# Performance work log

Hardware: AMD Instinct MI355X
Metric: run time of the kernel (lower is better)

The kernel has to match this reference:

```python
import jax, jax.numpy as jnp
import numpy as np

VOXEL_SCALE = 20.0   # cfg.SPARSE3D.VOXEL_SCALE (metric -> voxel pixels)
POOLER_SCALE = 0.25  # cfg.MODEL.ROI_BOX_HEAD.POOLER_SCALES_SPATIAL[0]
RES = 7              # pooler resolution per axis
EPS = 1e-5           # BatchNorm eps


def _roi_align_3d(feat, boxes_px, batch_idx, res):
    """3D ROIAlign, sampling_ratio=1 (one trilinear sample per bin).
    feat: [B, X, Y, Z, C] channels-last; boxes_px: [N,6] = (x1,y1,z1,x2,y2,z2)
    in feature-map coordinates. Returns [N, C, res, res, res]."""
    B, X, Y, Z, C = feat.shape
    N = boxes_px.shape[0]
    start, end = boxes_px[:, :3], boxes_px[:, 3:]
    size = jnp.maximum(end - start, 1.0)            # [N,3] legacy min roi size
    binsz = size / res
    off = jnp.arange(res, dtype=boxes_px.dtype) + 0.5
    px = start[:, 0:1] + off[None, :] * binsz[:, 0:1]   # [N,res]
    py = start[:, 1:2] + off[None, :] * binsz[:, 1:2]
    pz = start[:, 2:3] + off[None, :] * binsz[:, 2:3]
    P = res * res * res
    PX = jnp.broadcast_to(px[:, :, None, None], (N, res, res, res)).reshape(N, P)
    PY = jnp.broadcast_to(py[:, None, :, None], (N, res, res, res)).reshape(N, P)
    PZ = jnp.broadcast_to(pz[:, None, None, :], (N, res, res, res)).reshape(N, P)

    def corners(p, dim):
        p0 = jnp.floor(p)
        frac = p - p0
        i0 = jnp.clip(p0.astype(jnp.int32), 0, dim - 1)
        i1 = jnp.clip(p0.astype(jnp.int32) + 1, 0, dim - 1)
        return i0, i1, frac

    x0, x1, lx = corners(PX, X)
    y0, y1, ly = corners(PY, Y)
    z0, z1, lz = corners(PZ, Z)
    feat_flat = feat.reshape(B * X * Y * Z, C)
    base = batch_idx.astype(jnp.int32)[:, None]          # [N,1]
    acc = jnp.zeros((N, P, C), feat.dtype)
    for dx in (0, 1):  # 8 trilinear corners; fixed small loop
        xi, wx = (x0, 1.0 - lx) if dx == 0 else (x1, lx)
        for dy in (0, 1):
            yi, wy = (y0, 1.0 - ly) if dy == 0 else (y1, ly)
            for dz in (0, 1):
                zi, wz = (z0, 1.0 - lz) if dz == 0 else (z1, lz)
                lin = ((base * X + xi) * Y + yi) * Z + zi  # [N,P]
                acc = acc + (wx * wy * wz)[:, :, None] * feat_flat[lin]
    pooled = acc.reshape(N, res, res, res, C)  # 1 sample per bin -> no avg
    return pooled.transpose(0, 4, 1, 2, 3)     # [N, C, rx, ry, rz]


def setup_inputs():
    key = jax.random.key(0)
    ks = jax.random.split(key, 8)
    B, C, X, Y, Z = 2, 128, 80, 80, 20
    N, rep = 1024, 128 * RES              # rep = OUT_CHANNELS * pooler_z = 896
    in_size = C * RES * RES * RES         # 43904
    features = jax.random.normal(ks[0], (B, X, Y, Z, C), jnp.float32)
    ext = jnp.array([16.0, 16.0, 4.0], jnp.float32)  # metric extent = dim/(voxel_scale*pooler_scale)
    ctr = jax.random.uniform(ks[1], (N, 3), jnp.float32) * ext
    half = 0.25 + jax.random.uniform(ks[2], (N, 3), jnp.float32) * 1.75
    boxes = jnp.concatenate([ctr - half, ctr + half], axis=1)  # metric units
    batch_idx = jax.random.randint(ks[3], (N,), 0, B, jnp.int32)
    conv_w = jax.random.normal(ks[4], (rep, C, RES), jnp.float32) * 0.02
    conv_b = jnp.zeros((rep,), jnp.float32)
    gamma = jnp.ones((rep,), jnp.float32)
    beta = jnp.zeros((rep,), jnp.float32)
    fc6_w = jax.random.normal(ks[5], (in_size, rep), jnp.float32) * np.float32(1.0 / np.sqrt(in_size))
    fc6_b = jnp.zeros((rep,), jnp.float32)
    fc7_w = jax.random.normal(ks[6], (rep, rep), jnp.float32) * np.float32(1.0 / np.sqrt(rep))
    fc7_b = jnp.zeros((rep,), jnp.float32)
    return dict(features=features, boxes=boxes, conv_w=conv_w, conv_b=conv_b,
                gamma=gamma, beta=beta, fc6_w=fc6_w, fc6_b=fc6_b,
                fc7_w=fc7_w, fc7_b=fc7_b, batch_idx=batch_idx)


def reference(features, boxes, conv_w, conv_b, gamma, beta,
              fc6_w, fc6_b, fc7_w, fc7_b, batch_idx):
    # convert_metric_to_pixel (x voxel_scale) fused with pooler spatial scale
    boxes_px = boxes * (VOXEL_SCALE * POOLER_SCALE)
    pooled = _roi_align_3d(features, boxes_px, batch_idx, RES)  # [N,C,7,7,7]
    # conv3d kernel [1,1,Z]: contract channels and z -> [N, rep, 7, 7]
    y = jnp.einsum('ncxyz,rcz->nrxy', pooled, conv_w) + conv_b[None, :, None, None]
    # BatchNorm3d, training-mode batch statistics per channel
    mu = y.mean(axis=(0, 2, 3), keepdims=True)
    var = ((y - mu) ** 2).mean(axis=(0, 2, 3), keepdims=True)
    y = (y - mu) * jax.lax.rsqrt(var + EPS) * gamma[None, :, None, None] + beta[None, :, None, None]
    y = jax.nn.relu(y)
    x2 = y.reshape(y.shape[0], -1)                   # [N, rep*49] == [N, C*343]
    x3 = jax.nn.relu(x2 @ fc6_w + fc6_b)
    x4 = jax.nn.relu(x3 @ fc7_w + fc7_b)
    return x4
```

## Files before the change

kernel.cpp:

```cpp
#include <hip/hip_runtime.h>
#include <cstdint>

typedef unsigned short u16;
using bf16x8  = __attribute__((ext_vector_type(8))) __bf16;
using floatx4 = __attribute__((ext_vector_type(4))) float;

__device__ __forceinline__ u16 f2bf(float f) {
    uint32_t u = __builtin_bit_cast(uint32_t, f);
    u += 0x7fffu + ((u >> 16) & 1u);
    return (u16)(u >> 16);
}
__device__ __forceinline__ float bf2f(u16 h) {
    uint32_t u = ((uint32_t)h) << 16;
    return __builtin_bit_cast(float, u);
}

__global__ __launch_bounds__(256) void k_roialign(
    const float* __restrict__ feat, const float* __restrict__ boxes,
    const int* __restrict__ bidx, u16* __restrict__ A1)
{
    const int n = blockIdx.x;
    const int t = threadIdx.x;
    const float s = 5.0f;
    const float x1 = boxes[n*6+0]*s, y1 = boxes[n*6+1]*s, z1 = boxes[n*6+2]*s;
    const float x2 = boxes[n*6+3]*s, y2 = boxes[n*6+4]*s, z2 = boxes[n*6+5]*s;
    const float binx = fmaxf(x2-x1, 1.0f) * (1.0f/7.0f);
    const float biny = fmaxf(y2-y1, 1.0f) * (1.0f/7.0f);
    const float binz = fmaxf(z2-z1, 1.0f) * (1.0f/7.0f);
    const int b = bidx[n];
    const float* fb = feat + (size_t)b * 80 * 80 * 20 * 128;
    const int c4   = (t & 31) * 4;
    const int slot = t >> 5;

    for (int p = slot; p < 343; p += 8) {
        const int xq = p / 49;
        const int rem = p - xq * 49;
        const int yq = rem / 7;
        const int zq = rem - yq * 7;
        const float px = x1 + ((float)xq + 0.5f) * binx;
        const float py = y1 + ((float)yq + 0.5f) * biny;
        const float pz = z1 + ((float)zq + 0.5f) * binz;
        const float fx = floorf(px), fy = floorf(py), fz = floorf(pz);
        const float lx = px - fx, ly = py - fy, lz = pz - fz;
        const int xi0 = min(max((int)fx,     0), 79);
        const int xi1 = min(max((int)fx + 1, 0), 79);
        const int yi0 = min(max((int)fy,     0), 79);
        const int yi1 = min(max((int)fy + 1, 0), 79);
        const int zi0 = min(max((int)fz,     0), 19);
        const int zi1 = min(max((int)fz + 1, 0), 19);
        const float wx0 = 1.f-lx, wy0 = 1.f-ly, wz0 = 1.f-lz;
        const float w00 = wx0*wy0, w01 = wx0*ly, w10 = lx*wy0, w11 = lx*ly;
        float a0=0.f, a1=0.f, a2=0.f, a3=0.f;
#define RC(W, XI, YI, ZI) { \
        const float4 v = *(const float4*)(fb + (size_t)(((XI)*80+(YI))*20+(ZI))*128 + c4); \
        a0 = fmaf((W), v.x, a0); a1 = fmaf((W), v.y, a1); \
        a2 = fmaf((W), v.z, a2); a3 = fmaf((W), v.w, a3); }
        RC(w00*wz0, xi0, yi0, zi0); RC(w00*lz, xi0, yi0, zi1);
        RC(w01*wz0, xi0, yi1, zi0); RC(w01*lz, xi0, yi1, zi1);
        RC(w10*wz0, xi1, yi0, zi0); RC(w10*lz, xi1, yi0, zi1);
        RC(w11*wz0, xi1, yi1, zi0); RC(w11*lz, xi1, yi1, zi1);
#undef RC
        const int m = n * 49 + xq * 7 + yq;
        ushort4 o;
        o.x = f2bf(a0); o.y = f2bf(a1); o.z = f2bf(a2); o.w = f2bf(a3);
        *(ushort4*)(A1 + (size_t)m * 896 + zq * 128 + c4) = o;
    }
}

__global__ __launch_bounds__(256) void k_prep_wc(
    const float* __restrict__ w, u16* __restrict__ out)
{
    const int i = blockIdx.x * 256 + threadIdx.x;
    const int r = i / 896, k = i % 896;
    const int z = k >> 7, c = k & 127;
    out[i] = f2bf(w[(r * 128 + c) * 7 + z]);
}

template <int PERM>
__global__ __launch_bounds__(256) void k_transpose(
    const float* __restrict__ in, u16* __restrict__ out, int Kin)
{
    __shared__ u16 tile[64][72];
    const int kp0 = blockIdx.x * 64, r0 = blockIdx.y * 64;
    const int t = threadIdx.x;
#pragma unroll
    for (int it = 0; it < 16; ++it) {
        const int idx = it * 256 + t;
        const int i = idx >> 6, rl = idx & 63;
        const int kp = kp0 + i;
        const int k = PERM ? (kp % 896) * 49 + (kp / 896) : kp;
        tile[i][rl] = f2bf(in[(size_t)k * 896 + r0 + rl]);
    }
    __syncthreads();
#pragma unroll
    for (int it = 0; it < 16; ++it) {
        const int idx = it * 256 + t;
        const int rl = idx >> 6, i = idx & 63;
        out[(size_t)(r0 + rl) * Kin + kp0 + i] = tile[i][rl];
    }
}

template <int EPI>
__global__ __launch_bounds__(256) void k_gemm(
    const u16* __restrict__ A, const u16* __restrict__ Bt,
    float* __restrict__ outF, u16* __restrict__ outH,
    const float* __restrict__ bias, float* __restrict__ bnsum, float* __restrict__ bnsq,
    int Astride, int Bstride, int kpc, int ktot, int partStride)
{
    __shared__ __align__(16) u16 lA[128 * 40];
    __shared__ __align__(16) u16 lB[128 * 40];
    const int t = threadIdx.x;
    const int wave = t >> 6, lane = t & 63;
    const int wm = wave & 1, wn = wave >> 1;
    const int quad = lane >> 4, lr = lane & 15;
    const size_t m0 = (size_t)blockIdx.x * 128;
    const size_t n0 = (size_t)blockIdx.y * 128;
    const int kbeg = blockIdx.z * kpc;
    const int kend = min(kbeg + kpc, ktot);

    floatx4 acc[4][4];
    const floatx4 zero = {0.f, 0.f, 0.f, 0.f};
#pragma unroll
    for (int a = 0; a < 4; ++a)
#pragma unroll
        for (int bq = 0; bq < 4; ++bq) acc[a][bq] = zero;

    const int e0 = t * 8;
    const int r0s = e0 >> 5, c0s = e0 & 31;
    const int e1 = e0 + 2048;
    const int r1s = e1 >> 5, c1s = e1 & 31;
    const u16* Ab = A + m0 * (size_t)Astride;
    const u16* Bb = Bt + n0 * (size_t)Bstride;

    for (int ks = kbeg; ks < kend; ++ks) {
        const size_t k0 = (size_t)ks * 32;
        const uint4 va0 = *(const uint4*)(Ab + (size_t)r0s * Astride + k0 + c0s);
        const uint4 va1 = *(const uint4*)(Ab + (size_t)r1s * Astride + k0 + c1s);
        const uint4 vb0 = *(const uint4*)(Bb + (size_t)r0s * Bstride + k0 + c0s);
        const uint4 vb1 = *(const uint4*)(Bb + (size_t)r1s * Bstride + k0 + c1s);
        __syncthreads();
        *(uint4*)(lA + r0s * 40 + c0s) = va0;
        *(uint4*)(lA + r1s * 40 + c1s) = va1;
        *(uint4*)(lB + r0s * 40 + c0s) = vb0;
        *(uint4*)(lB + r1s * 40 + c1s) = vb1;
        __syncthreads();
        bf16x8 af[4], bfr[4];
#pragma unroll
        for (int mt = 0; mt < 4; ++mt)
            af[mt] = *(const bf16x8*)(lA + (wm * 64 + mt * 16 + lr) * 40 + quad * 8);
#pragma unroll
        for (int nt = 0; nt < 4; ++nt)
            bfr[nt] = *(const bf16x8*)(lB + (wn * 64 + nt * 16 + lr) * 40 + quad * 8);
#pragma unroll
        for (int mt = 0; mt < 4; ++mt)
#pragma unroll
            for (int nt = 0; nt < 4; ++nt)
                acc[mt][nt] = __builtin_amdgcn_mfma_f32_16x16x32_bf16(
                    af[mt], bfr[nt], acc[mt][nt], 0, 0, 0);
    }

    if (EPI == 0) {
#pragma unroll
        for (int nt = 0; nt < 4; ++nt) {
            const int n = (int)n0 + wn * 64 + nt * 16 + lr;
            const float bv = bias[n];
            float s1 = 0.f, s2 = 0.f;
#pragma unroll
            for (int mt = 0; mt < 4; ++mt) {
#pragma unroll
                for (int j = 0; j < 4; ++j) {
                    const int m = (int)m0 + wm * 64 + mt * 16 + quad * 4 + j;
                    const float v = acc[mt][nt][j] + bv;
                    outH[(size_t)m * 896 + n] = f2bf(v);
                    s1 += v;
                    s2 = fmaf(v, v, s2);
                }
            }
            s1 += __shfl_xor(s1, 16); s1 += __shfl_xor(s1, 32);
            s2 += __shfl_xor(s2, 16); s2 += __shfl_xor(s2, 32);
            if (quad == 0) {
                atomicAdd(&bnsum[n], s1);
                atomicAdd(&bnsq[n],  s2);
            }
        }
    } else {
        float* po = outF + (size_t)blockIdx.z * partStride;
#pragma unroll
        for (int nt = 0; nt < 4; ++nt) {
            const int n = (int)n0 + wn * 64 + nt * 16 + lr;
#pragma unroll
            for (int mt = 0; mt < 4; ++mt) {
#pragma unroll
                for (int j = 0; j < 4; ++j) {
                    const int m = (int)m0 + wm * 64 + mt * 16 + quad * 4 + j;
                    po[(size_t)m * 896 + n] = acc[mt][nt][j];
                }
            }
        }
    }
}

__global__ __launch_bounds__(256) void k_bn_apply(
    u16* __restrict__ y, const float* __restrict__ s1, const float* __restrict__ s2,
    const float* __restrict__ gamma, const float* __restrict__ beta)
{
    const size_t i = ((size_t)blockIdx.x * 256 + threadIdx.x) * 8;
    uint4 d = *(const uint4*)(y + i);
    const u16* h = (const u16*)&d;
    const int r0 = (int)(i % 896);
    __align__(16) u16 o[8];
    const float invM = 1.0f / 50176.0f;
#pragma unroll
    for (int j = 0; j < 8; ++j) {
        const int r = r0 + j;
        const float mu  = s1[r] * invM;
        const float var = fmaf(-mu, mu, s2[r] * invM);
        const float rs  = rsqrtf(var + 1e-5f);
        const float v   = (bf2f(h[j]) - mu) * rs * gamma[r] + beta[r];
        o[j] = f2bf(fmaxf(v, 0.f));
    }
    *(uint4*)(y + i) = *(const uint4*)o;
}

__global__ __launch_bounds__(256) void k_x3(
    const float* __restrict__ part, const float* __restrict__ bias, u16* __restrict__ x3)
{
    const size_t i = ((size_t)blockIdx.x * 256 + threadIdx.x) * 4;
    float a0=0.f, a1=0.f, a2=0.f, a3=0.f;
#pragma unroll
    for (int c = 0; c < 16; ++c) {
        const float4 v = *(const float4*)(part + (size_t)c * 917504 + i);
        a0 += v.x; a1 += v.y; a2 += v.z; a3 += v.w;
    }
    const int r = (int)(i % 896);
    ushort4 o;
    o.x = f2bf(fmaxf(a0 + bias[r+0], 0.f));
    o.y = f2bf(fmaxf(a1 + bias[r+1], 0.f));
    o.z = f2bf(fmaxf(a2 + bias[r+2], 0.f));
    o.w = f2bf(fmaxf(a3 + bias[r+3], 0.f));
    *(ushort4*)(x3 + i) = o;
}

__global__ __launch_bounds__(256) void k_out(
    const float* __restrict__ part, const float* __restrict__ bias, float* __restrict__ out)
{
    const size_t i = ((size_t)blockIdx.x * 256 + threadIdx.x) * 4;
    float a0=0.f, a1=0.f, a2=0.f, a3=0.f;
#pragma unroll
    for (int c = 0; c < 4; ++c) {
        const float4 v = *(const float4*)(part + (size_t)c * 917504 + i);
        a0 += v.x; a1 += v.y; a2 += v.z; a3 += v.w;
    }
    const int r = (int)(i % 896);
    float4 o;
    o.x = fmaxf(a0 + bias[r+0], 0.f);
    o.y = fmaxf(a1 + bias[r+1], 0.f);
    o.z = fmaxf(a2 + bias[r+2], 0.f);
    o.w = fmaxf(a3 + bias[r+3], 0.f);
    *(float4*)(out + i) = o;
}

extern "C" void kernel_launch(void* const* d_in, const int* in_sizes, int n_in,
                              void* d_out, int out_size, void* d_ws, size_t ws_size,
                              hipStream_t stream)
{
    (void)in_sizes; (void)n_in; (void)out_size; (void)ws_size;
    const float* features = (const float*)d_in[0];
    const float* boxes    = (const float*)d_in[1];
    const float* conv_w   = (const float*)d_in[2];
    const float* conv_b   = (const float*)d_in[3];
    const float* gamma    = (const float*)d_in[4];
    const float* beta     = (const float*)d_in[5];
    const float* fc6_w    = (const float*)d_in[6];
    const float* fc6_b    = (const float*)d_in[7];
    const float* fc7_w    = (const float*)d_in[8];
    const float* fc7_b    = (const float*)d_in[9];
    const int*   batch_idx = (const int*)d_in[10];
    float* out = (float*)d_out;
    char* ws = (char*)d_ws;

    size_t off = 0;
    auto alloc = [&](size_t b) { size_t o = off; off += (b + 255) & ~(size_t)255; return o; };
    const size_t oA1   = alloc(50176ull * 896 * 2);
    const size_t oWcT  = alloc(896ull * 896 * 2);
    const size_t oY    = alloc(50176ull * 896 * 2);
    const size_t oF6T  = alloc(43904ull * 896 * 2);
    const size_t oF7T  = alloc(896ull * 896 * 2);
    const size_t oStat = alloc(8192);
    const size_t oP2 = oA1;
    const size_t oX3 = oA1 + 58720256;
    const size_t oP3 = oX3 + 1835008;

    u16*   A1    = (u16*)(ws + oA1);
    u16*   WcT   = (u16*)(ws + oWcT);
    u16*   Y     = (u16*)(ws + oY);
    u16*   F6T   = (u16*)(ws + oF6T);
    u16*   F7T   = (u16*)(ws + oF7T);
    float* bnsum = (float*)(ws + oStat);
    float* bnsq  = bnsum + 1024;
    float* P2    = (float*)(ws + oP2);
    u16*   X3    = (u16*)(ws + oX3);
    float* P3    = (float*)(ws + oP3);

    k_prep_wc<<<3136, 256, 0, stream>>>(conv_w, WcT);
    k_transpose<1><<<dim3(686, 14), 256, 0, stream>>>(fc6_w, F6T, 43904);
    k_transpose<0><<<dim3(14, 14), 256, 0, stream>>>(fc7_w, F7T, 896);
    hipMemsetAsync(ws + oStat, 0, 8192, stream);

    k_roialign<<<1024, 256, 0, stream>>>(features, boxes, batch_idx, A1);

    k_gemm<0><<<dim3(392, 7, 1), 256, 0, stream>>>(
        A1, WcT, nullptr, Y, conv_b, bnsum, bnsq, 896, 896, 28, 28, 0);

    k_bn_apply<<<21952, 256, 0, stream>>>(Y, bnsum, bnsq, gamma, beta);

    k_gemm<1><<<dim3(8, 7, 16), 256, 0, stream>>>(
        Y, F6T, P2, nullptr, nullptr, nullptr, nullptr, 43904, 43904, 86, 1372, 917504);
    k_x3<<<896, 256, 0, stream>>>(P2, fc6_b, X3);

    k_gemm<1><<<dim3(8, 7, 4), 256, 0, stream>>>(
        X3, F7T, P3, nullptr, nullptr, nullptr, nullptr, 896, 896, 7, 28, 917504);
    k_out<<<896, 256, 0, stream>>>(P3, fc7_b, out);
}
```

Baseline: 824.2 us.

## Load GEMM tiles directly to LDS with XOR swizzle and swap grid order

Replaces the register-staged global loads plus LDS stores in the GEMM kernel with direct global-to-LDS loads (global_load_lds, 16 bytes per lane). The padded LDS layout becomes an unpadded 32-wide layout with an XOR swizzle to avoid bank conflicts on the fragment reads. Grid dimensions are swapped so blocks sharing the same A rows are adjacent, which may improve L2 reuse of A. The aim is to cut register traffic and VGPR pressure in the load path. The risk lies in getting the swizzle and the direct-to-LDS addressing correct.

```diff
diff --git a/kernel.cpp b/kernel.cpp
--- a/kernel.cpp
+++ b/kernel.cpp
@@ -13,6 +13,12 @@
 __device__ __forceinline__ float bf2f(u16 h) {
     uint32_t u = ((uint32_t)h) << 16;
     return __builtin_bit_cast(float, u);
+}
+
+__device__ __forceinline__ void gl2lds16(const u16* g, u16* l) {
+    __builtin_amdgcn_global_load_lds(
+        (const __attribute__((address_space(1))) uint32_t*)g,
+        (__attribute__((address_space(3))) uint32_t*)l, 16, 0, 0);
 }
 
 __global__ __launch_bounds__(256) void k_roialign(
@@ -107,14 +113,14 @@
     const float* __restrict__ bias, float* __restrict__ bnsum, float* __restrict__ bnsq,
     int Astride, int Bstride, int kpc, int ktot, int partStride)
 {
-    __shared__ __align__(16) u16 lA[128 * 40];
-    __shared__ __align__(16) u16 lB[128 * 40];
+    __shared__ __align__(16) u16 lA[128 * 32];
+    __shared__ __align__(16) u16 lB[128 * 32];
     const int t = threadIdx.x;
     const int wave = t >> 6, lane = t & 63;
     const int wm = wave & 1, wn = wave >> 1;
     const int quad = lane >> 4, lr = lane & 15;
-    const size_t m0 = (size_t)blockIdx.x * 128;
-    const size_t n0 = (size_t)blockIdx.y * 128;
+    const size_t n0 = (size_t)blockIdx.x * 128;
+    const size_t m0 = (size_t)blockIdx.y * 128;
     const int kbeg = blockIdx.z * kpc;
     const int kend = min(kbeg + kpc, ktot);
 
@@ -125,32 +131,37 @@
 #pragma unroll
         for (int bq = 0; bq < 4; ++bq) acc[a][bq] = zero;
 
-    const int e0 = t * 8;
-    const int r0s = e0 >> 5, c0s = e0 & 31;
-    const int e1 = e0 + 2048;
-    const int r1s = e1 >> 5, c1s = e1 & 31;
+    const int rs0 = wave * 32 + (lane >> 2);
+    const int rs1 = rs0 + 16;
+    const int qsw = (lane & 3) ^ ((lane >> 2) & 3);
     const u16* Ab = A + m0 * (size_t)Astride;
     const u16* Bb = Bt + n0 * (size_t)Bstride;
+    const u16* srcA0 = Ab + (size_t)rs0 * Astride + qsw * 8;
+    const u16* srcA1 = Ab + (size_t)rs1 * Astride + qsw * 8;
+    const u16* srcB0 = Bb + (size_t)rs0 * Bstride + qsw * 8;
+    const u16* srcB1 = Bb + (size_t)rs1 * Bstride + qsw * 8;
+    u16* ldsA0 = lA + (wave * 2 + 0) * 512;
+    u16* ldsA1 = lA + (wave * 2 + 1) * 512;
+    u16* ldsB0 = lB + (wave * 2 + 0) * 512;
+    u16* ldsB1 = lB + (wave * 2 + 1) * 512;
+
+    const int fsw = (quad ^ (lr & 3)) * 8;
 
     for (int ks = kbeg; ks < kend; ++ks) {
         const size_t k0 = (size_t)ks * 32;
-        const uint4 va0 = *(const uint4*)(Ab + (size_t)r0s * Astride + k0 + c0s);
-        const uint4 va1 = *(const uint4*)(Ab + (size_t)r1s * Astride + k0 + c1s);
-        const uint4 vb0 = *(const uint4*)(Bb + (size_t)r0s * Bstride + k0 + c0s);
-        const uint4 vb1 = *(const uint4*)(Bb + (size_t)r1s * Bstride + k0 + c1s);
         __syncthreads();
-        *(uint4*)(lA + r0s * 40 + c0s) = va0;
-        *(uint4*)(lA + r1s * 40 + c1s) = va1;
-        *(uint4*)(lB + r0s * 40 + c0s) = vb0;
-        *(uint4*)(lB + r1s * 40 + c1s) = vb1;
+        gl2lds16(srcA0 + k0, ldsA0);
+        gl2lds16(srcA1 + k0, ldsA1);
+        gl2lds16(srcB0 + k0, ldsB0);
+        gl2lds16(srcB1 + k0, ldsB1);
         __syncthreads();
         bf16x8 af[4], bfr[4];
 #pragma unroll
         for (int mt = 0; mt < 4; ++mt)
-            af[mt] = *(const bf16x8*)(lA + (wm * 64 + mt * 16 + lr) * 40 + quad * 8);
+            af[mt] = *(const bf16x8*)(lA + (wm * 64 + mt * 16 + lr) * 32 + fsw);
 #pragma unroll
         for (int nt = 0; nt < 4; ++nt)
-            bfr[nt] = *(const bf16x8*)(lB + (wn * 64 + nt * 16 + lr) * 40 + quad * 8);
+            bfr[nt] = *(const bf16x8*)(lB + (wn * 64 + nt * 16 + lr) * 32 + fsw);
 #pragma unroll
         for (int mt = 0; mt < 4; ++mt)
 #pragma unroll
@@ -309,16 +320,16 @@
 
     k_roialign<<<1024, 256, 0, stream>>>(features, boxes, batch_idx, A1);
 
-    k_gemm<0><<<dim3(392, 7, 1), 256, 0, stream>>>(
+    k_gemm<0><<<dim3(7, 392, 1), 256, 0, stream>>>(
         A1, WcT, nullptr, Y, conv_b, bnsum, bnsq, 896, 896, 28, 28, 0);
 
     k_bn_apply<<<21952, 256, 0, stream>>>(Y, bnsum, bnsq, gamma, beta);
 
-    k_gemm<1><<<dim3(8, 7, 16), 256, 0, stream>>>(
+    k_gemm<1><<<dim3(7, 8, 16), 256, 0, stream>>>(
         Y, F6T, P2, nullptr, nullptr, nullptr, nullptr, 43904, 43904, 86, 1372, 917504);
     k_x3<<<896, 256, 0, stream>>>(P2, fc6_b, X3);
 
-    k_gemm<1><<<dim3(8, 7, 4), 256, 0, stream>>>(
+    k_gemm<1><<<dim3(7, 8, 4), 256, 0, stream>>>(
         X3, F7T, P3, nullptr, nullptr, nullptr, nullptr, 896, 896, 7, 28, 917504);
     k_out<<<896, 256, 0, stream>>>(P3, fc7_b, out);
 }
```

Result: slower. 883.4 us (+7.2%).
